# Kernel tuning notes

Hardware: AMD Instinct MI355X
Metric: run time of the kernel (lower is better)

## Reference

```python
import jax, jax.numpy as jnp
import numpy as np

B, S, D, P, H = 32, 1024, 512, 720, 4   # batch, seq_len (=codebook_size), enc_in, pred_len, heads
COMMIT_W, ORTHO_W = 1.0, 0.8


def setup_inputs() -> dict:
    key = jax.random.key(0)
    ks = jax.random.split(key, 6)
    return {
        "x": jax.random.normal(ks[0], (B, S, D), jnp.float32),
        "w_in": jax.random.normal(ks[1], (H * D, D), jnp.float32) * 0.02,   # project_in: dim -> heads*dim
        "b_in": jnp.zeros((H * D,), jnp.float32),
        "embed": jax.random.normal(ks[2], (H, S, D), jnp.float32),          # per-head codebook [h, C, d]
        "w_out": jax.random.normal(ks[3], (D, H * D), jnp.float32) * 0.02,  # project_out: heads*dim -> dim
        "b_out": jnp.zeros((D,), jnp.float32),
        "w_lin": jax.random.normal(ks[4], (P, S), jnp.float32) * 0.02,      # Linear over time axis
        "b_lin": jnp.zeros((P,), jnp.float32),
    }


def reference(x, w_in, b_in, embed, w_out, b_out, w_lin, b_lin):
    C = embed.shape[1]
    # Normalization: subtract last timestep (detached)
    seq_last = jax.lax.stop_gradient(x[:, -1:, :])          # [B,1,D]
    x0 = x - seq_last                                       # [B,S,D]

    # --- VectorQuantize ---
    xi = x0 @ w_in.T + b_in                                 # [B,S,H*D] project_in
    # 'b n (h d) -> h (b n) d' (separate codebook per head)
    f = xi.reshape(B, S, H, D).transpose(2, 0, 1, 3).reshape(H, B * S, D)
    # squared-euclidean distances to codes: [H, B*S, C]
    d2 = (jnp.sum(f * f, -1, keepdims=True)
          - 2.0 * jnp.einsum('hnd,hcd->hnc', f, embed)
          + jnp.sum(embed * embed, -1)[:, None, :])
    ind = jnp.argmin(d2, axis=-1)                           # [H, B*S]
    q = jnp.take_along_axis(embed, ind[:, :, None], axis=1)  # gather -> [H, B*S, D]

    # commitment loss (learnable codebook => quantize NOT detached)
    commit_loss = jnp.mean((q - f) ** 2)
    # orthogonal regularization on full codebook
    normed = embed / jnp.linalg.norm(embed, axis=-1, keepdims=True)
    cs = jnp.einsum('hid,hjd->hij', normed, normed)         # [H,C,C]
    ortho_loss = jnp.sum(cs ** 2) / (H * C * C) - 1.0 / C
    loss = COMMIT_W * commit_loss + ORTHO_W * ortho_loss

    # straight-through estimator
    q_st = f + jax.lax.stop_gradient(q - f)
    # 'h (b n) d -> b n (h d)'
    qo = q_st.reshape(H, B, S, D).transpose(1, 2, 0, 3).reshape(B, S, H * D)
    quantized = qo @ w_out.T + b_out                        # [B,S,D] project_out

    # Linear over the time axis: permute(0,2,1) -> Linear(S->P) -> permute back
    y = jnp.einsum('bnd,pn->bpd', quantized, w_lin) + b_lin[None, :, None]
    y = y + seq_last                                        # [B,P,D]

    indices = ind.reshape(H, B, S).transpose(1, 2, 0)       # [B,S,H]
    return y, indices, loss
```

## Files before the change

kernel.cpp:

```cpp
#include <hip/hip_runtime.h>
#include <stdint.h>

typedef unsigned int u32;
typedef unsigned long long u64;
typedef _Float16 f16;
typedef __attribute__((ext_vector_type(8))) _Float16 f16x8;
typedef __attribute__((ext_vector_type(4))) _Float16 f16x4;
typedef __attribute__((ext_vector_type(2))) _Float16 f16x2;
typedef __attribute__((ext_vector_type(4))) float f32x4;

#define MFMA16(a, b, c) __builtin_amdgcn_mfma_f32_16x16x32_f16((a), (b), (c), 0, 0, 0)
#define MARGIN 2.0f
#define WAITV(n) asm volatile("s_waitcnt vmcnt(" #n ")" ::: "memory")

__device__ __forceinline__ u32 ford(float x) { u32 u = __float_as_uint(x); return (u & 0x80000000u) ? ~u : (u | 0x80000000u); }
__device__ __forceinline__ float iford(u32 v) { u32 u = (v & 0x80000000u) ? (v & 0x7FFFFFFFu) : ~v; return __uint_as_float(u); }
__device__ __forceinline__ int xswz(int i, int n) { return (i & 7) * (n >> 3) + (i >> 3); }

typedef __attribute__((address_space(1))) const unsigned char ga_t;
typedef __attribute__((address_space(3))) unsigned char la_t;
__device__ __forceinline__ void gl16(const void* g, void* l) {
  __builtin_amdgcn_global_load_lds((ga_t*)g, (la_t*)l, 16, 0, 0);
}

template <int LDK>
__device__ __forceinline__ void stg8k(const f16* gRowBase, int ktile, char* sdst, int tid) {
#pragma unroll
  for (int it = 0; it < 2; ++it) {
    const int u = (tid + (it << 8)) << 4;
    const int r = u >> 6, s = (u >> 4) & 3;
    const char* src = (const char*)gRowBase + (size_t)r * (LDK * 2) + ((size_t)ktile << 6) +
                      (size_t)((s ^ ((r >> 1) & 3)) << 4);
    gl16(src, sdst + u);
  }
}

template <int MODE>
__global__ __launch_bounds__(256, (MODE == 0 || MODE == 3) ? 2 : 3) void gemm2(
    const f16* __restrict__ Ah, const f16* __restrict__ Al,
    const f16* __restrict__ Bh, const f16* __restrict__ Bl,
    int chrows,
    void* __restrict__ out0, void* __restrict__ out1,
    const float* __restrict__ bias, const float* __restrict__ aux,
    u64* __restrict__ slots) {
  constexpr bool K1 = (MODE == 0);
  constexpr int LDK = (MODE == 2 || MODE == 4) ? 1024 : 512;
  constexpr int OPS = K1 ? 4 : 2;
  constexpr int D = K1 ? 2 : 3;
  constexpr int KT = (MODE == 2 || MODE == 4) ? 32 : 16;
  constexpr int BUF = OPS * 8192;
  constexpr int LDS_SZ = D * BUF + ((MODE == 3) ? 8704 : 0);
  __shared__ char lds[LDS_SZ];

  const int tid = threadIdx.x;
  const int lane = tid & 63, wid = tid >> 6;
  const int wm = wid >> 1, wn = wid & 1;

  int blkm, blkn, z = 0;
  {
    const int s = xswz(blockIdx.x, gridDim.x);
    if constexpr (MODE == 0) { blkn = s & 15; blkm = s >> 4; }
    else if constexpr (MODE == 1) { blkn = s & 3; blkm = s >> 2; z = blkm >> 3; }
    else if constexpr (MODE == 2) { blkn = s & 3; blkm = (s >> 2) & 3; z = s >> 4; }
    else if constexpr (MODE == 3) {
      const int bph = (chrows >> 7) << 3;
      z = s / bph;
      const int rem = s - z * bph;
      blkm = rem >> 3; blkn = rem & 7;
    } else { const int r2 = s % 24; blkm = r2 % 6; blkn = r2 / 6; z = s / 24; }
  }

  if constexpr (MODE == 3) {
    u64* candL = (u64*)(lds + D * BUF);
    int* cntL = (int*)(lds + D * BUF + 8192);
    for (int i = tid; i < 1024; i += 256) candL[i] = ~0ull;
    if (tid < 128) cntL[tid] = 0;
  }

  const f16 *Ab, *Bb, *Alb = nullptr, *Blb = nullptr;
  if constexpr (MODE == 0) {
    Ab = Ah + (size_t)blkm * 65536;
    Alb = Al + (size_t)blkm * 65536;
    Bb = Bh + (size_t)blkn * 65536;
    Blb = Bl + (size_t)blkn * 65536;
  } else if constexpr (MODE == 1) {
    Ab = Ah + (size_t)blkm * 65536;
    Bb = Bh + (size_t)z * 262144 + (size_t)blkn * 65536;
  } else if constexpr (MODE == 2) {
    Ab = Ah + (size_t)z * 524288 + (size_t)blkm * 131072;
    Bb = Bh + (size_t)z * 524288 + (size_t)blkn * 131072;
  } else if constexpr (MODE == 3) {
    Ab = Ah + ((size_t)z * chrows + (size_t)blkm * 128) * 512;
    Bb = Bh + (size_t)z * 524288 + (size_t)blkn * 65536;
  } else {
    Ab = Ah + (size_t)blkm * 131072;
    Bb = Bh + (size_t)z * 524288 + (size_t)blkn * 131072;
  }

  f32x4 acc[4][4];
#pragma unroll
  for (int i = 0; i < 4; ++i)
#pragma unroll
    for (int j = 0; j < 4; ++j) acc[i][j] = f32x4{0.f, 0.f, 0.f, 0.f};

#pragma unroll
  for (int d = 0; d < D - 1; ++d) {
    char* nb = lds + d * BUF;
    stg8k<LDK>(Ab, d, nb, tid);
    if constexpr (K1) stg8k<LDK>(Alb, d, nb + 8192, tid);
    stg8k<LDK>(Bb, d, nb + (K1 ? 16384 : 8192), tid);
    if constexpr (K1) stg8k<LDK>(Blb, d, nb + 24576, tid);
  }

#pragma unroll
  for (int kc = 0; kc < KT; ++kc) {
    if (kc + D - 1 < KT) {
      char* nb = lds + ((kc + D - 1) % D) * BUF;
      stg8k<LDK>(Ab, kc + D - 1, nb, tid);
      if constexpr (K1) stg8k<LDK>(Alb, kc + D - 1, nb + 8192, tid);
      stg8k<LDK>(Bb, kc + D - 1, nb + (K1 ? 16384 : 8192), tid);
      if constexpr (K1) stg8k<LDK>(Blb, kc + D - 1, nb + 24576, tid);
    }
    const int nf = KT - 1 - kc;
    if (nf >= D - 1) WAITV(8);
    else if (D == 3 && nf == 1) WAITV(4);
    else WAITV(0);
    __builtin_amdgcn_s_barrier();
    const char* cbuf = lds + (kc % D) * BUF;
    f16x8 ah[4], al[4];
#pragma unroll
    for (int mt = 0; mt < 4; ++mt) {
      const int rr = wm * 64 + mt * 16 + (lane & 15);
      const int o = rr * 64 + (((lane >> 4) ^ ((rr >> 1) & 3)) << 4);
      ah[mt] = *(const f16x8*)(cbuf + o);
      if constexpr (K1) al[mt] = *(const f16x8*)(cbuf + 8192 + o);
    }
    __builtin_amdgcn_s_setprio(1);
#pragma unroll
    for (int nt = 0; nt < 4; ++nt) {
      const int rn = wn * 64 + nt * 16 + (lane & 15);
      const int o = rn * 64 + (((lane >> 4) ^ ((rn >> 1) & 3)) << 4);
      const f16x8 bh = *(const f16x8*)(cbuf + (K1 ? 16384 : 8192) + o);
      f16x8 bl;
      if constexpr (K1) bl = *(const f16x8*)(cbuf + 24576 + o);
#pragma unroll
      for (int mt = 0; mt < 4; ++mt) {
        if constexpr (K1) {
          acc[mt][nt] = MFMA16(al[mt], bh, acc[mt][nt]);
          acc[mt][nt] = MFMA16(ah[mt], bl, acc[mt][nt]);
        }
        acc[mt][nt] = MFMA16(ah[mt], bh, acc[mt][nt]);
      }
    }
    __builtin_amdgcn_s_setprio(0);
    __builtin_amdgcn_s_barrier();
  }

  if constexpr (MODE == 0) {
    f16* fh = (f16*)out0;
    f16* fl = (f16*)out1;
#pragma unroll
    for (int nt = 0; nt < 4; ++nt) {
      const int gc = blkn * 128 + wn * 64 + nt * 16 + (lane & 15);
      const float bv = bias[gc];
      const int h = gc >> 9, d = gc & 511;
#pragma unroll
      for (int mt = 0; mt < 4; ++mt)
#pragma unroll
        for (int r = 0; r < 4; ++r) {
          const int grow = blkm * 128 + wm * 64 + mt * 16 + ((lane >> 4) << 2) + r;
          const float v = acc[mt][nt][r] * 6.103515625e-05f + bv;
          const f16 hv = (f16)v;
          const size_t off = ((size_t)h * chrows + grow) * 512 + d;
          fh[off] = hv;
          fl[off] = (f16)(v - (float)hv);
        }
    }
  } else if constexpr (MODE == 1) {
    f16* o = (f16*)out0;
#pragma unroll
    for (int nt = 0; nt < 4; ++nt) {
      const int gc = blkn * 128 + wn * 64 + nt * 16 + (lane & 15);
#pragma unroll
      for (int mt = 0; mt < 4; ++mt)
#pragma unroll
        for (int r = 0; r < 4; ++r) {
          const size_t grow = (size_t)blkm * 128 + wm * 64 + mt * 16 + ((lane >> 4) << 2) + r;
          o[grow * 512 + gc] = (f16)acc[mt][nt][r];
        }
    }
  } else if constexpr (MODE == 2) {
    float ssum = 0.f;
#pragma unroll
    for (int mt = 0; mt < 4; ++mt)
#pragma unroll
      for (int nt = 0; nt < 4; ++nt)
#pragma unroll
        for (int r = 0; r < 4; ++r) ssum += acc[mt][nt][r] * acc[mt][nt][r];
#pragma unroll
    for (int o = 1; o < 64; o <<= 1) ssum += __shfl_xor(ssum, o);
    float* wp = (float*)lds;
    __syncthreads();
    if (lane == 0) wp[wid] = ssum;
    __syncthreads();
    if (tid == 0) {
      const float p = wp[0] + wp[1] + wp[2] + wp[3];
      atomicAdd(slots + (blockIdx.x & 63), (u64)llrintf(p * 16777216.f));
    }
  } else if constexpr (MODE == 3) {
    u64* candL = (u64*)(lds + D * BUF);
    int* cntL = (int*)(lds + D * BUF + 8192);
    u64* candG = (u64*)out0;
    const int h = z;
    float escol[4];
    int cc[4];
#pragma unroll
    for (int nt = 0; nt < 4; ++nt) {
      cc[nt] = blkn * 128 + wn * 64 + nt * 16 + (lane & 15);
      escol[nt] = aux[h * 1024 + cc[nt]];
    }
#pragma unroll
    for (int mt = 0; mt < 4; ++mt)
#pragma unroll
      for (int r = 0; r < 4; ++r) {
        const int row_l = wm * 64 + mt * 16 + ((lane >> 4) << 2) + r;
        float vals[4];
        float mn = 3.4e38f;
#pragma unroll
        for (int nt = 0; nt < 4; ++nt) {
          const float v = escol[nt] - 2.0f * acc[mt][nt][r];
          vals[nt] = v;
          mn = fminf(mn, v);
        }
#pragma unroll
        for (int o = 1; o < 16; o <<= 1) mn = fminf(mn, __shfl_xor(mn, o));
        const float lim = mn + MARGIN;
#pragma unroll
        for (int nt = 0; nt < 4; ++nt)
          if (vals[nt] <= lim) {
            const int p = atomicAdd(&cntL[row_l], 1);
            if (p < 8) candL[(row_l << 3) + p] = ((u64)ford(vals[nt]) << 32) | (u32)cc[nt];
          }
      }
    __syncthreads();
#pragma unroll
    for (int j = 0; j < 4; ++j) {
      const int idx = tid * 4 + j;
      const int row_l = idx >> 3, slot = idx & 7;
      const size_t grow = (size_t)blkm * 128 + row_l;
      candG[((size_t)h * chrows + grow) * 64 + (size_t)blkn * 8 + slot] = candL[idx];
    }
  } else {
    float* oy = (float*)out0 + (size_t)z * 368640;
    const float* xseq = aux + (size_t)z * 524288 + 523776;
    float sl[4];
    int gd[4];
#pragma unroll
    for (int nt = 0; nt < 4; ++nt) {
      gd[nt] = blkn * 128 + wn * 64 + nt * 16 + (lane & 15);
      sl[nt] = xseq[gd[nt]];
    }
#pragma unroll
    for (int mt = 0; mt < 4; ++mt)
#pragma unroll
      for (int r = 0; r < 4; ++r) {
        const int p = blkm * 128 + wm * 64 + mt * 16 + ((lane >> 4) << 2) + r;
        if (p < 720) {
          const float bp = bias[p];
#pragma unroll
          for (int nt = 0; nt < 4; ++nt) oy[(size_t)p * 512 + gd[nt]] = acc[mt][nt][r] + bp + sl[nt];
        }
      }
  }
}

__global__ __launch_bounds__(256, 4) void rescore_k(
    const u64* __restrict__ candG, const f16* __restrict__ fh,
    const f16* __restrict__ fl, const float* __restrict__ embed,
    int n0, int shCH,
    int* __restrict__ indw, float* __restrict__ indout, u64* __restrict__ cslots) {
  const int tid = threadIdx.x, lane = tid & 63, wid = tid >> 6;
  const int r = blockIdx.x * 4 + wid;
  const int h = r >> shCH, row = r & ((1 << shCH) - 1);
  u64 cu = candG[(size_t)r * 64 + lane];
  u64 mn = cu;
#pragma unroll
  for (int o = 1; o < 64; o <<= 1) { const u64 t = __shfl_xor(mn, o); if (t < mn) mn = t; }
  const float lim = iford((u32)(mn >> 32)) + MARGIN;
  const bool pass = iford((u32)(cu >> 32)) <= lim;
  u64 mask = __ballot(pass);
  float fv[8];
  {
    const size_t fo = (size_t)r * 512 + lane * 8;
    const f16x8 hv = *(const f16x8*)(fh + fo);
    const f16x8 lv = *(const f16x8*)(fl + fo);
#pragma unroll
    for (int j = 0; j < 8; ++j) fv[j] = (float)hv[j] + (float)lv[j];
  }
  double bestd = 1e300;
  int bestc = 0x7FFFFFFF;
  while (mask) {
    const int src = __ffsll((unsigned long long)mask) - 1;
    mask &= mask - 1;
    const int c = (int)(u32)__shfl(cu, src);
    const float* e = embed + ((size_t)h * 1024 + c) * 512 + lane * 8;
    const float4 e0 = *(const float4*)e, e1 = *(const float4*)(e + 4);
    const float ev[8] = {e0.x, e0.y, e0.z, e0.w, e1.x, e1.y, e1.z, e1.w};
    double sd = 0.0;
#pragma unroll
    for (int j = 0; j < 8; ++j) { const double d = (double)fv[j] - (double)ev[j]; sd += d * d; }
#pragma unroll
    for (int o = 1; o < 64; o <<= 1) sd += __shfl_xor(sd, o);
    if (sd < bestd || (sd == bestd && c < bestc)) { bestd = sd; bestc = c; }
  }
  if (lane == 0) {
    const int n = n0 + row;
    indw[(size_t)n * 4 + h] = bestc;
    indout[(size_t)n * 4 + h] = (float)bestc;
    atomicAdd(cslots + (blockIdx.x & 255), (u64)llrint(bestd * 65536.0));
  }
}

__global__ __launch_bounds__(256) void quantize_qT(
    const int* __restrict__ indw, const f16* __restrict__ Ep,
    const float* __restrict__ b_out, f16* __restrict__ qT) {
  const int tid = threadIdx.x;
  const int b = blockIdx.x >> 4, s0 = (blockIdx.x & 15) << 6;
  __shared__ int inds[64][4];
  inds[tid >> 2][tid & 3] = indw[(size_t)(b * 1024 + s0 + (tid >> 2)) * 4 + (tid & 3)];
  __syncthreads();
  const int d0 = tid * 2;
  const float ba0 = b_out[d0], ba1 = b_out[d0 + 1];
  u32 r0[32], r1[32];
  f16 t0 = (f16)0.f, t1 = (f16)0.f;
#pragma unroll
  for (int ss = 0; ss < 64; ++ss) {
    float a0 = ba0, a1 = ba1;
#pragma unroll
    for (int h = 0; h < 4; ++h) {
      const int c = inds[ss][h];
      const f16x2 p = *(const f16x2*)(Ep + (((size_t)h * 1024 + c) * 512 + d0));
      a0 += (float)p[0];
      a1 += (float)p[1];
    }
    const f16 q0 = (f16)a0, q1 = (f16)a1;
    if (ss & 1) {
      f16x2 w0; w0[0] = t0; w0[1] = q0; __builtin_memcpy(&r0[ss >> 1], &w0, 4);
      f16x2 w1; w1[0] = t1; w1[1] = q1; __builtin_memcpy(&r1[ss >> 1], &w1, 4);
    } else { t0 = q0; t1 = q1; }
  }
  const size_t o0 = ((size_t)b * 512 + d0) * 1024 + s0;
#pragma unroll
  for (int i = 0; i < 8; ++i) {
    uint4 v; v.x = r0[4 * i]; v.y = r0[4 * i + 1]; v.z = r0[4 * i + 2]; v.w = r0[4 * i + 3];
    *(uint4*)(qT + o0 + (size_t)i * 8) = v;
  }
  const size_t o1 = o0 + 1024;
#pragma unroll
  for (int i = 0; i < 8; ++i) {
    uint4 v; v.x = r1[4 * i]; v.y = r1[4 * i + 1]; v.z = r1[4 * i + 2]; v.w = r1[4 * i + 3];
    *(uint4*)(qT + o1 + (size_t)i * 8) = v;
  }
}

__global__ __launch_bounds__(256) void prep_x0(const float* __restrict__ x, int n0,
                                               f16* __restrict__ ht, f16* __restrict__ lt) {
  const int id = blockIdx.x * 256 + threadIdx.x;
  const int k8 = id & 63, r = id >> 6;
  const int n = n0 + r, b = n >> 10;
  const float* ap = x + (size_t)n * 512 + k8 * 8;
  const float* sp = x + (size_t)b * 524288 + 523776 + k8 * 8;
  const float4 a0 = *(const float4*)ap, a1 = *(const float4*)(ap + 4);
  const float4 s0 = *(const float4*)sp, s1 = *(const float4*)(sp + 4);
  const float v[8] = {(a0.x - s0.x) * 16.f, (a0.y - s0.y) * 16.f, (a0.z - s0.z) * 16.f,
                      (a0.w - s0.w) * 16.f, (a1.x - s1.x) * 16.f, (a1.y - s1.y) * 16.f,
                      (a1.z - s1.z) * 16.f, (a1.w - s1.w) * 16.f};
  f16x8 hv, lv;
#pragma unroll
  for (int j = 0; j < 8; ++j) { const f16 h = (f16)v[j]; hv[j] = h; lv[j] = (f16)(v[j] - (float)h); }
  const size_t off = (size_t)r * 512 + k8 * 8;
  *(f16x8*)(ht + off) = hv;
  *(f16x8*)(lt + off) = lv;
}

__global__ __launch_bounds__(256) void prep_win(const float* __restrict__ src,
                                                f16* __restrict__ hi, f16* __restrict__ lo) {
  const size_t e = ((size_t)blockIdx.x * 256 + threadIdx.x) * 4;
  const float4 v = *(const float4*)(src + e);
  const float w[4] = {v.x * 1024.f, v.y * 1024.f, v.z * 1024.f, v.w * 1024.f};
  f16x4 hv, lv;
#pragma unroll
  for (int j = 0; j < 4; ++j) { const f16 h = (f16)w[j]; hv[j] = h; lv[j] = (f16)(w[j] - (float)h); }
  *(f16x4*)(hi + e) = hv;
  *(f16x4*)(lo + e) = lv;
}

__global__ __launch_bounds__(256) void prep_embed_k(const float* __restrict__ em,
                                                    f16* __restrict__ ef,
                                                    float* __restrict__ esq,
                                                    float* __restrict__ invn) {
  const int tid = threadIdx.x, lane = tid & 63, wid = tid >> 6;
  const int row = blockIdx.x * 4 + wid;
  const float* er = em + (size_t)row * 512 + lane * 8;
  const float4 a = *(const float4*)er, b = *(const float4*)(er + 4);
  f16x8 v;
  v[0] = (f16)a.x; v[1] = (f16)a.y; v[2] = (f16)a.z; v[3] = (f16)a.w;
  v[4] = (f16)b.x; v[5] = (f16)b.y; v[6] = (f16)b.z; v[7] = (f16)b.w;
  *(f16x8*)(ef + (size_t)row * 512 + lane * 8) = v;
  float s = a.x * a.x + a.y * a.y + a.z * a.z + a.w * a.w +
            b.x * b.x + b.y * b.y + b.z * b.z + b.w * b.w;
#pragma unroll
  for (int o = 1; o < 64; o <<= 1) s += __shfl_xor(s, o);
  if (lane == 0) { esq[row] = s; invn[row] = 1.0f / sqrtf(s); }
}

__global__ __launch_bounds__(256) void prep_wout(const float* __restrict__ src,
                                                 f16* __restrict__ dst) {
  const int id = blockIdx.x * 256 + threadIdx.x;
  const int k8 = id & 63, rg = id >> 6;
  const int d = rg & 511, h = rg >> 9;
  const float* ap = src + (size_t)d * 2048 + h * 512 + k8 * 8;
  const float4 a0 = *(const float4*)ap, a1 = *(const float4*)(ap + 4);
  f16x8 v;
  v[0] = (f16)a0.x; v[1] = (f16)a0.y; v[2] = (f16)a0.z; v[3] = (f16)a0.w;
  v[4] = (f16)a1.x; v[5] = (f16)a1.y; v[6] = (f16)a1.z; v[7] = (f16)a1.w;
  *(f16x8*)(dst + (size_t)h * 262144 + (size_t)d * 512 + k8 * 8) = v;
}

__global__ __launch_bounds__(256) void prep_wlin(const float* __restrict__ src,
                                                 f16* __restrict__ dst) {
  const int id = blockIdx.x * 256 + threadIdx.x;
  const int k8 = id & 127, row = id >> 7;
  float4 a0 = {0.f, 0.f, 0.f, 0.f}, a1 = a0;
  if (row < 720) {
    const float* ap = src + (size_t)row * 1024 + k8 * 8;
    a0 = *(const float4*)ap;
    a1 = *(const float4*)(ap + 4);
  }
  f16x8 v;
  v[0] = (f16)a0.x; v[1] = (f16)a0.y; v[2] = (f16)a0.z; v[3] = (f16)a0.w;
  v[4] = (f16)a1.x; v[5] = (f16)a1.y; v[6] = (f16)a1.z; v[7] = (f16)a1.w;
  *(f16x8*)(dst + (size_t)row * 1024 + k8 * 8) = v;
}

__global__ __launch_bounds__(256) void prep_normT(const float* __restrict__ em,
                                                  const float* __restrict__ invn,
                                                  f16* __restrict__ nT) {
  __shared__ float t[64 * 65];
  const int tid = threadIdx.x;
  const int bx = blockIdx.x;
  const int h = bx >> 7, rem = bx & 127, cb = rem >> 3, db = rem & 7;
  const int c0 = cb * 64, d0 = db * 64;
  const int j = tid & 63, i0 = tid >> 6;
#pragma unroll
  for (int p = 0; p < 16; ++p) {
    const int i = p * 4 + i0;
    t[i * 65 + j] = em[(size_t)h * 524288 + (size_t)(c0 + i) * 512 + d0 + j] * invn[h * 1024 + c0 + i];
  }
  __syncthreads();
#pragma unroll
  for (int p = 0; p < 16; ++p) {
    const int i = p * 4 + i0;
    nT[(size_t)h * 524288 + (size_t)(d0 + i) * 1024 + c0 + j] = (f16)t[j * 65 + i];
  }
}

__global__ void finalize_k(const u64* __restrict__ cs, const u64* __restrict__ gs,
                           float* __restrict__ out) {
  const int lane = threadIdx.x;
  u64 c = cs[lane] + cs[lane + 64] + cs[lane + 128] + cs[lane + 192];
  u64 g = gs[lane];
#pragma unroll
  for (int o = 1; o < 64; o <<= 1) {
    c += __shfl_xor(c, o);
    g += __shfl_xor(g, o);
  }
  if (lane == 0) {
    const double commit = (double)c / 65536.0 / 67108864.0;
    const double ortho = (double)g / 16777216.0 / 4194304.0 - (1.0 / 1024.0);
    out[11927552] = (float)(commit + 0.8 * ortho);
  }
}

__global__ void ws_fail_k(float* out) {
  if (threadIdx.x == 0) out[11927552] = -777777.0f;
}

extern "C" void kernel_launch(void* const* d_in, const int* in_sizes, int n_in,
                              void* d_out, int out_size, void* d_ws, size_t ws_size,
                              hipStream_t stream) {
  (void)in_sizes; (void)n_in; (void)out_size;
  const float* x = (const float*)d_in[0];
  const float* w_in = (const float*)d_in[1];
  const float* b_in = (const float*)d_in[2];
  const float* embed = (const float*)d_in[3];
  const float* w_out = (const float*)d_in[4];
  const float* b_out = (const float*)d_in[5];
  const float* w_lin = (const float*)d_in[6];
  const float* b_lin = (const float*)d_in[7];
  float* out = (float*)d_out;
  char* ws = (char*)d_ws;

  constexpr size_t SZ_WIN = 2097152, SZ_EFT = 4194304, SZ_WOUT = 2097152;
  constexpr size_t SZ_EP = 4194304, SZ_WLIN = 1572864, SZ_NT = 4194304;
  constexpr size_t SZ_SMALL = 16384 + 16384 + 524288 + 2048 + 512;
  constexpr size_t FIXED = SZ_WIN * 2 + SZ_EFT + SZ_WOUT + SZ_EP + SZ_WLIN + SZ_NT + SZ_SMALL;

  int CH = 16384, shCH = 14;
  if (ws_size < FIXED + (size_t)16384 * 12288) { CH = 8192; shCH = 13; }
  if (ws_size < FIXED + (size_t)CH * 12288) {
    ws_fail_k<<<1, 64, 0, stream>>>(out);
    return;
  }

  size_t off = 0;
  f16* x0h = (f16*)(ws + off); off += (size_t)CH * 1024;
  f16* x0l = (f16*)(ws + off); off += (size_t)CH * 1024;
  f16* fh = (f16*)(ws + off); off += (size_t)CH * 4096;
  f16* fl = (f16*)(ws + off); off += (size_t)CH * 4096;
  u64* cand = (u64*)(ws + off); off += (size_t)CH * 2048;
  f16* winh = (f16*)(ws + off); off += SZ_WIN;
  f16* winl = (f16*)(ws + off); off += SZ_WIN;
  f16* eft = (f16*)(ws + off); off += SZ_EFT;
  f16* wout = (f16*)(ws + off); off += SZ_WOUT;
  f16* Ep = (f16*)(ws + off); off += SZ_EP;
  f16* wlint = (f16*)(ws + off); off += SZ_WLIN;
  f16* nT = (f16*)(ws + off); off += SZ_NT;
  float* esq = (float*)(ws + off); off += 16384;
  float* invn = (float*)(ws + off); off += 16384;
  int* indw = (int*)(ws + off); off += 524288;
  u64* cslots = (u64*)(ws + off); off += 2048;
  u64* gslots = (u64*)(ws + off); off += 512;
  f16* qT = (f16*)ws;

  hipMemsetAsync((void*)cslots, 0, 2560, stream);

  prep_win<<<1024, 256, 0, stream>>>(w_in, winh, winl);
  prep_embed_k<<<1024, 256, 0, stream>>>(embed, eft, esq, invn);
  prep_normT<<<512, 256, 0, stream>>>(embed, invn, nT);
  prep_wout<<<512, 256, 0, stream>>>(w_out, wout);
  prep_wlin<<<384, 256, 0, stream>>>(w_lin, wlint);

  gemm2<1><<<128, 256, 0, stream>>>(eft, nullptr, wout, nullptr, 0,
                                    Ep, nullptr, nullptr, nullptr, nullptr);
  gemm2<2><<<64, 256, 0, stream>>>(nT, nullptr, nT, nullptr, 0,
                                   nullptr, nullptr, nullptr, nullptr, gslots);

  for (int c0 = 0; c0 < 32768; c0 += CH) {
    prep_x0<<<CH / 4, 256, 0, stream>>>(x, c0, x0h, x0l);
    gemm2<0><<<(CH / 128) * 16, 256, 0, stream>>>(x0h, x0l, winh, winl, CH,
                                                  fh, fl, b_in, nullptr, nullptr);
    gemm2<3><<<(CH / 128) * 32, 256, 0, stream>>>(fh, nullptr, eft, nullptr, CH,
                                                  cand, nullptr, nullptr, esq, nullptr);
    rescore_k<<<CH, 256, 0, stream>>>(cand, fh, fl, embed, c0, shCH,
                                      indw, out + 11796480, cslots);
  }

  quantize_qT<<<512, 256, 0, stream>>>(indw, Ep, b_out, qT);
  gemm2<4><<<768, 256, 0, stream>>>(wlint, nullptr, qT, nullptr, 0,
                                    out, nullptr, b_lin, x, nullptr);
  finalize_k<<<1, 64, 0, stream>>>(cslots, gslots, out);
}
```

Baseline: 708.3 us.

## Enlarge distance GEMM tile to 256 rows and write candidates directly to global

The codebook-distance GEMM (MODE 3) now computes a 256x128 tile per block with 8 M-subtiles per wave, so each staged codebook tile is reused across twice as many feature rows. The LDS candidate staging buffer is removed: candidates go straight to global memory, which a hipMemsetAsync pre-fills with 0xFF instead of the in-kernel initialisation. Register pressure goes up (128 accumulator floats per lane) and an extra memset per chunk is added, which may hurt occupancy or add launch overhead.

```diff
diff --git a/kernel.cpp b/kernel.cpp
--- a/kernel.cpp
+++ b/kernel.cpp
@@ -44,12 +44,13 @@
     const float* __restrict__ bias, const float* __restrict__ aux,
     u64* __restrict__ slots) {
   constexpr bool K1 = (MODE == 0);
+  constexpr bool SC = (MODE == 3);
   constexpr int LDK = (MODE == 2 || MODE == 4) ? 1024 : 512;
-  constexpr int OPS = K1 ? 4 : 2;
   constexpr int D = K1 ? 2 : 3;
   constexpr int KT = (MODE == 2 || MODE == 4) ? 32 : 16;
-  constexpr int BUF = OPS * 8192;
-  constexpr int LDS_SZ = D * BUF + ((MODE == 3) ? 8704 : 0);
+  constexpr int MT = SC ? 8 : 4;
+  constexpr int BUF = K1 ? 32768 : (SC ? 24576 : 16384);
+  constexpr int LDS_SZ = D * BUF + (SC ? 1024 : 0);
   __shared__ char lds[LDS_SZ];
 
   const int tid = threadIdx.x;
@@ -63,19 +64,15 @@
     else if constexpr (MODE == 1) { blkn = s & 3; blkm = s >> 2; z = blkm >> 3; }
     else if constexpr (MODE == 2) { blkn = s & 3; blkm = (s >> 2) & 3; z = s >> 4; }
     else if constexpr (MODE == 3) {
-      const int bph = (chrows >> 7) << 3;
+      const int bph = (chrows >> 8) << 3;
       z = s / bph;
       const int rem = s - z * bph;
       blkm = rem >> 3; blkn = rem & 7;
     } else { const int r2 = s % 24; blkm = r2 % 6; blkn = r2 / 6; z = s / 24; }
   }
 
-  if constexpr (MODE == 3) {
-    u64* candL = (u64*)(lds + D * BUF);
-    int* cntL = (int*)(lds + D * BUF + 8192);
-    for (int i = tid; i < 1024; i += 256) candL[i] = ~0ull;
-    if (tid < 128) cntL[tid] = 0;
-  }
+  int* cntL = (int*)(lds + D * BUF);
+  if constexpr (SC) cntL[tid] = 0;
 
   const f16 *Ab, *Bb, *Alb = nullptr, *Blb = nullptr;
   if constexpr (MODE == 0) {
@@ -90,47 +87,52 @@
     Ab = Ah + (size_t)z * 524288 + (size_t)blkm * 131072;
     Bb = Bh + (size_t)z * 524288 + (size_t)blkn * 131072;
   } else if constexpr (MODE == 3) {
-    Ab = Ah + ((size_t)z * chrows + (size_t)blkm * 128) * 512;
+    Ab = Ah + ((size_t)z * chrows + (size_t)blkm * 256) * 512;
     Bb = Bh + (size_t)z * 524288 + (size_t)blkn * 65536;
   } else {
     Ab = Ah + (size_t)blkm * 131072;
     Bb = Bh + (size_t)z * 524288 + (size_t)blkn * 131072;
   }
 
-  f32x4 acc[4][4];
-#pragma unroll
-  for (int i = 0; i < 4; ++i)
+  f32x4 acc[MT][4];
+#pragma unroll
+  for (int i = 0; i < MT; ++i)
 #pragma unroll
     for (int j = 0; j < 4; ++j) acc[i][j] = f32x4{0.f, 0.f, 0.f, 0.f};
 
-#pragma unroll
-  for (int d = 0; d < D - 1; ++d) {
-    char* nb = lds + d * BUF;
-    stg8k<LDK>(Ab, d, nb, tid);
-    if constexpr (K1) stg8k<LDK>(Alb, d, nb + 8192, tid);
-    stg8k<LDK>(Bb, d, nb + (K1 ? 16384 : 8192), tid);
-    if constexpr (K1) stg8k<LDK>(Blb, d, nb + 24576, tid);
-  }
+  auto stage = [&](int kt, char* nb) {
+    stg8k<LDK>(Ab, kt, nb, tid);
+    if constexpr (SC) stg8k<LDK>(Ab + 65536, kt, nb + 8192, tid);
+    if constexpr (K1) stg8k<LDK>(Alb, kt, nb + 8192, tid);
+    stg8k<LDK>(Bb, kt, nb + 16384 - (SC || K1 ? 0 : 8192), tid);
+    if constexpr (K1) stg8k<LDK>(Blb, kt, nb + 24576, tid);
+  };
+
+#pragma unroll
+  for (int d = 0; d < D - 1; ++d) stage(d, lds + d * BUF);
 
 #pragma unroll
   for (int kc = 0; kc < KT; ++kc) {
-    if (kc + D - 1 < KT) {
-      char* nb = lds + ((kc + D - 1) % D) * BUF;
-      stg8k<LDK>(Ab, kc + D - 1, nb, tid);
-      if constexpr (K1) stg8k<LDK>(Alb, kc + D - 1, nb + 8192, tid);
-      stg8k<LDK>(Bb, kc + D - 1, nb + (K1 ? 16384 : 8192), tid);
-      if constexpr (K1) stg8k<LDK>(Blb, kc + D - 1, nb + 24576, tid);
-    }
+    if (kc + D - 1 < KT) stage(kc + D - 1, lds + ((kc + D - 1) % D) * BUF);
     const int nf = KT - 1 - kc;
-    if (nf >= D - 1) WAITV(8);
-    else if (D == 3 && nf == 1) WAITV(4);
-    else WAITV(0);
+    if constexpr (SC) {
+      if (nf >= 2) WAITV(12);
+      else if (nf == 1) WAITV(6);
+      else WAITV(0);
+    } else if constexpr (K1) {
+      if (nf >= 1) WAITV(8);
+      else WAITV(0);
+    } else {
+      if (nf >= 2) WAITV(8);
+      else if (nf == 1) WAITV(4);
+      else WAITV(0);
+    }
     __builtin_amdgcn_s_barrier();
     const char* cbuf = lds + (kc % D) * BUF;
-    f16x8 ah[4], al[4];
-#pragma unroll
-    for (int mt = 0; mt < 4; ++mt) {
-      const int rr = wm * 64 + mt * 16 + (lane & 15);
+    f16x8 ah[MT], al[4];
+#pragma unroll
+    for (int mt = 0; mt < MT; ++mt) {
+      const int rr = wm * (MT * 16) + mt * 16 + (lane & 15);
       const int o = rr * 64 + (((lane >> 4) ^ ((rr >> 1) & 3)) << 4);
       ah[mt] = *(const f16x8*)(cbuf + o);
       if constexpr (K1) al[mt] = *(const f16x8*)(cbuf + 8192 + o);
@@ -140,11 +142,11 @@
     for (int nt = 0; nt < 4; ++nt) {
       const int rn = wn * 64 + nt * 16 + (lane & 15);
       const int o = rn * 64 + (((lane >> 4) ^ ((rn >> 1) & 3)) << 4);
-      const f16x8 bh = *(const f16x8*)(cbuf + (K1 ? 16384 : 8192) + o);
+      const f16x8 bh = *(const f16x8*)(cbuf + (K1 || SC ? 16384 : 8192) + o);
       f16x8 bl;
       if constexpr (K1) bl = *(const f16x8*)(cbuf + 24576 + o);
 #pragma unroll
-      for (int mt = 0; mt < 4; ++mt) {
+      for (int mt = 0; mt < MT; ++mt) {
         if constexpr (K1) {
           acc[mt][nt] = MFMA16(al[mt], bh, acc[mt][nt]);
           acc[mt][nt] = MFMA16(ah[mt], bl, acc[mt][nt]);
@@ -208,8 +210,6 @@
       atomicAdd(slots + (blockIdx.x & 63), (u64)llrintf(p * 16777216.f));
     }
   } else if constexpr (MODE == 3) {
-    u64* candL = (u64*)(lds + D * BUF);
-    int* cntL = (int*)(lds + D * BUF + 8192);
     u64* candG = (u64*)out0;
     const int h = z;
     float escol[4];
@@ -220,10 +220,10 @@
       escol[nt] = aux[h * 1024 + cc[nt]];
     }
 #pragma unroll
-    for (int mt = 0; mt < 4; ++mt)
+    for (int mt = 0; mt < 8; ++mt)
 #pragma unroll
       for (int r = 0; r < 4; ++r) {
-        const int row_l = wm * 64 + mt * 16 + ((lane >> 4) << 2) + r;
+        const int row_l = wm * 128 + mt * 16 + ((lane >> 4) << 2) + r;
         float vals[4];
         float mn = 3.4e38f;
 #pragma unroll
@@ -239,17 +239,13 @@
         for (int nt = 0; nt < 4; ++nt)
           if (vals[nt] <= lim) {
             const int p = atomicAdd(&cntL[row_l], 1);
-            if (p < 8) candL[(row_l << 3) + p] = ((u64)ford(vals[nt]) << 32) | (u32)cc[nt];
+            if (p < 8) {
+              const size_t grow = (size_t)blkm * 256 + row_l;
+              candG[(((size_t)h * chrows + grow) * 8 + blkn) * 8 + p] =
+                  ((u64)ford(vals[nt]) << 32) | (u32)cc[nt];
+            }
           }
       }
-    __syncthreads();
-#pragma unroll
-    for (int j = 0; j < 4; ++j) {
-      const int idx = tid * 4 + j;
-      const int row_l = idx >> 3, slot = idx & 7;
-      const size_t grow = (size_t)blkm * 128 + row_l;
-      candG[((size_t)h * chrows + grow) * 64 + (size_t)blkn * 8 + slot] = candL[idx];
-    }
   } else {
     float* oy = (float*)out0 + (size_t)z * 368640;
     const float* xseq = aux + (size_t)z * 524288 + 523776;
@@ -550,7 +546,8 @@
     prep_x0<<<CH / 4, 256, 0, stream>>>(x, c0, x0h, x0l);
     gemm2<0><<<(CH / 128) * 16, 256, 0, stream>>>(x0h, x0l, winh, winl, CH,
                                                   fh, fl, b_in, nullptr, nullptr);
-    gemm2<3><<<(CH / 128) * 32, 256, 0, stream>>>(fh, nullptr, eft, nullptr, CH,
+    hipMemsetAsync((void*)cand, 0xFF, (size_t)CH * 2048, stream);
+    gemm2<3><<<(CH / 256) * 32, 256, 0, stream>>>(fh, nullptr, eft, nullptr, CH,
                                                   cand, nullptr, nullptr, esq, nullptr);
     rescore_k<<<CH, 256, 0, stream>>>(cand, fh, fl, embed, c0, shCH,
                                       indw, out + 11796480, cslots);
```

Result: no change. 698.7 us (-1.4%).
